# Performance work log

Hardware: AMD Instinct MI355X
Metric: run time of the kernel (lower is better)

Reference implementation:

```python
import jax, jax.numpy as jnp
import numpy as np

MAX_REL = 127  # default max_relative_position of NEZHA-style RelativePositionsEncoding


def rel_pos_encoding(L, d):
    """Clipped relative-distance sinusoidal encoding, shape [L, L, d]."""
    vocab = 2 * MAX_REL + 1
    pos = np.arange(vocab, dtype=np.float32)[:, None]
    i = np.arange(d)
    div = np.power(10000.0, (2 * (i // 2)) / d).astype(np.float32)
    ang = pos / div
    table = np.where(i % 2 == 0, np.sin(ang), np.cos(ang)).astype(np.float32)  # [vocab, d]
    dist = np.clip(np.arange(L)[None, :] - np.arange(L)[:, None], -MAX_REL, MAX_REL) + MAX_REL
    return jnp.asarray(table[dist])  # [L, L, d]


def setup_inputs() -> dict:
    key = jax.random.key(0)
    ks = jax.random.split(key, 5)
    B, L, H, C = 2, 256, 256, 5
    return {
        "hidden_state": jax.random.normal(ks[0], (B, L, H), dtype=jnp.float32),
        "mask": jnp.ones((B, L), dtype=jnp.int32),
        "Wh_w": jax.random.normal(ks[1], (4 * H, H), dtype=jnp.float32) * 0.02,
        "Wh_b": jax.random.normal(ks[2], (H,), dtype=jnp.float32) * 0.02,
        "Wo_w": jax.random.normal(ks[3], (H, C), dtype=jnp.float32) * 0.02,
        "Wo_b": jax.random.normal(ks[4], (C,), dtype=jnp.float32) * 0.02,
    }


def reference(hidden_state, mask, Wh_w, Wh_b, Wo_w, Wo_b):
    B, L, H = hidden_state.shape
    # Decompose Wh over the concat [end, start, end-start, end*start]:
    # Wh(cat) = end@(We+Wd) + start@(Ws-Wd) + (end*start)@Wm + rel@Wh + b  (exact, linearity)
    We, Ws, Wd, Wm = jnp.split(Wh_w, 4, axis=0)  # each [H, H]
    rel = rel_pos_encoding(L, 4 * H)                        # [L, L, 4H]
    rel_term = jnp.einsum('ijk,kh->ijh', rel, Wh_w)         # [L, L, H]
    a = hidden_state @ (We + Wd)                            # end-index contribution  [B, L, H]
    b = hidden_state @ (Ws - Wd)                            # start-index contribution [B, L, H]
    prod = hidden_state[:, :, None, :] * hidden_state[:, None, :, :]  # [B, L, L, H]
    pre = a[:, :, None, :] + b[:, None, :, :] + prod @ Wm + rel_term[None] + Wh_b
    hij = jnp.tanh(pre)                                     # [B, L, L, H]
    logits = hij @ Wo_w + Wo_b                              # [B, L, L, C]
    logits = jnp.transpose(logits, (0, 3, 1, 2))            # [B, C, L, L]
    m = mask.astype(bool)
    bad = (~m[:, None, :, None]) | (~m[:, None, None, :])
    logits = jnp.where(bad, -jnp.inf, logits)
    tri = jnp.tril(jnp.ones((L, L), logits.dtype), -1) * 1e12
    return logits - tri
```

## Files before the change

kernel.cpp:

```cpp
#include <hip/hip_runtime.h>
#include <math.h>

typedef _Float16 half8 __attribute__((ext_vector_type(8)));
typedef _Float16 half4v __attribute__((ext_vector_type(4)));
typedef float floatx4 __attribute__((ext_vector_type(4)));

union U16 { uint4 u; half8 h; };

__global__ __launch_bounds__(256) void k_prep1(
    const float* __restrict__ hs, const float* __restrict__ Wh,
    const float* __restrict__ Wo,
    float* __restrict__ Rp, float* __restrict__ ap, float* __restrict__ bp,
    uint4* __restrict__ WmT2, uint4* __restrict__ WoPk)
{
  __shared__ __align__(16) char pool[32768];
  int bid = blockIdx.x, tid = threadIdx.x;

  if (bid < 256) {
    float (*tbl)[8] = (float(*)[8])pool;
    int dg = bid >> 3, kq = bid & 7, d0 = dg * 8, k0 = kq * 128;
    for (int idx = tid; idx < 1024; idx += 256) {
      int t = idx >> 3, dl = idx & 7;
      int k = k0 + t;
      float e = (float)(k & ~1) * (1.0f / 1024.f);
      float div = powf(10000.f, e);
      float ang = (float)(d0 + dl) / div;
      tbl[t][dl] = (k & 1) ? cosf(ang) : sinf(ang);
    }
    __syncthreads();
    int h = tid;
    float acc[8] = {0, 0, 0, 0, 0, 0, 0, 0};
    for (int kk = 0; kk < 128; ++kk) {
      float wv = Wh[(k0 + kk) * 256 + h];
      float tr[8];
      *(float4*)&tr[0] = *(const float4*)&tbl[kk][0];
      *(float4*)&tr[4] = *(const float4*)&tbl[kk][4];
#pragma unroll
      for (int dl = 0; dl < 8; ++dl) acc[dl] = fmaf(tr[dl], wv, acc[dl]);
    }
#pragma unroll
    for (int dl = 0; dl < 8; ++dl)
      Rp[kq * 65536 + (d0 + dl) * 256 + h] = acc[dl];

  } else if (bid < 512) {
    float (*xs)[8] = (float(*)[8])pool;
    int g = bid - 256, rg = g >> 2, kq = g & 3;
    int r0 = rg * 8, k0 = kq * 64;
    for (int idx = tid; idx < 512; idx += 256) {
      int kk = idx >> 3, r = idx & 7;
      xs[kk][r] = hs[(r0 + r) * 256 + k0 + kk];
    }
    __syncthreads();
    int h = tid;
    float aa[8] = {0, 0, 0, 0, 0, 0, 0, 0}, bb[8] = {0, 0, 0, 0, 0, 0, 0, 0};
    for (int kk = 0; kk < 64; ++kk) {
      int k = k0 + kk;
      float we = Wh[k * 256 + h];
      float wsv = Wh[(256 + k) * 256 + h];
      float wd = Wh[(512 + k) * 256 + h];
      float wA = we + wd, wB = wsv - wd;
      float xr[8];
      *(float4*)&xr[0] = *(const float4*)&xs[kk][0];
      *(float4*)&xr[4] = *(const float4*)&xs[kk][4];
#pragma unroll
      for (int r = 0; r < 8; ++r) {
        aa[r] = fmaf(xr[r], wA, aa[r]);
        bb[r] = fmaf(xr[r], wB, bb[r]);
      }
    }
#pragma unroll
    for (int r = 0; r < 8; ++r) {
      ap[kq * 131072 + (r0 + r) * 256 + h] = aa[r];
      bp[kq * 131072 + (r0 + r) * 256 + h] = bb[r];
    }

  } else if (bid < 516) {
    _Float16 (*T)[256] = (_Float16(*)[256])pool;
    int q = bid - 512;
    for (int idx = tid; idx < 16384; idx += 256) {
      int k = idx >> 8, h = idx & 255;
      T[k][h] = (_Float16)Wh[(768 + q * 64 + k) * 256 + h];
    }
    __syncthreads();
    for (int gi = tid; gi < 2048; gi += 256) {
      int kbl = gi >> 8, h = gi & 255;
      U16 v;
#pragma unroll
      for (int e = 0; e < 8; ++e) v.h[e] = T[kbl * 8 + e][h];
      WmT2[(q * 8 + kbl) * 256 + h] = v.u;
    }

  } else {
    for (int gi = tid; gi < 512; gi += 256) {
      int kb = gi >> 4, c = gi & 15;
      U16 v;
#pragma unroll
      for (int e = 0; e < 8; ++e)
        v.h[e] = (c < 5) ? (_Float16)Wo[(kb * 8 + e) * 5 + c] : (_Float16)0.f;
      WoPk[gi] = v.u;
    }
  }
}

__global__ __launch_bounds__(256) void k_prep2(
    const float* __restrict__ Rp, const float* __restrict__ ap,
    const float* __restrict__ bp,
    float* __restrict__ R, float* __restrict__ a, float* __restrict__ bv)
{
  int bid = blockIdx.x, h = threadIdx.x;
  if (bid < 255) {
    int d = bid;
    float s = 0.f;
#pragma unroll
    for (int kq = 0; kq < 8; ++kq) s += Rp[kq * 65536 + d * 256 + h];
    R[d * 256 + h] = s;
  } else {
    int r0 = (bid - 255) * 2;
#pragma unroll
    for (int rr = 0; rr < 2; ++rr) {
      int r = r0 + rr;
      float sa = 0.f, sb = 0.f;
#pragma unroll
      for (int kq = 0; kq < 4; ++kq) {
        sa += ap[kq * 131072 + r * 256 + h];
        sb += bp[kq * 131072 + r * 256 + h];
      }
      a[r * 256 + h] = sa;
      bv[r * 256 + h] = sb;
    }
  }
}

__global__ __launch_bounds__(256, 4) void k_main(
    const float* __restrict__ hs, const int* __restrict__ mask,
    const float* __restrict__ R, const float* __restrict__ a,
    const float* __restrict__ bvec, const float* __restrict__ Whb,
    const uint4* __restrict__ WmT2, const uint4* __restrict__ WoPk,
    const float* __restrict__ Wob, float* __restrict__ out)
{
  __shared__ __align__(16) char smem[34304];
  _Float16 (*As)[264] = (_Float16(*)[264])smem;
  float (*stg)[268] = (float(*)[268])smem;

  int bid = blockIdx.x, tid = threadIdx.x;
  int jt = bid & 3, i = (bid >> 2) & 255, b = bid >> 10;
  int j0 = jt * 64;
  int lane = tid & 63, w = tid >> 6;
  int c16 = lane & 15, quad = lane >> 4;
  const float* hsb = hs + (size_t)b * 65536;

  float av[4];
#pragma unroll
  for (int ht2 = 0; ht2 < 4; ++ht2) {
    int hp = 64 * w + 16 * ht2 + c16;
    av[ht2] = a[((size_t)(b * 256 + i)) * 256 + hp] + Whb[hp];
  }

  floatx4 acc[4][4];
#pragma unroll
  for (int hf = 0; hf < 2; ++hf) {
    int jbase = j0 + hf * 32;
#pragma unroll
    for (int it = 0; it < 8; ++it) {
      int idx = it * 256 + tid;
      int row = idx >> 6;
      int c4 = (idx & 63) << 2;
      int jg = jbase + row;
      int dd = jg - i;
      dd = dd < -127 ? -127 : (dd > 127 ? 127 : dd);
      dd += 127;
      float4 bb = *(const float4*)(bvec + ((size_t)(b * 256 + jg)) * 256 + c4);
      float4 rr = *(const float4*)(R + (size_t)dd * 256 + c4);
      float4 s;
      s.x = bb.x + rr.x; s.y = bb.y + rr.y;
      s.z = bb.z + rr.z; s.w = bb.w + rr.w;
      *(float4*)&stg[row][c4] = s;
    }
    __syncthreads();
#pragma unroll
    for (int jj = 0; jj < 2; ++jj) {
      int jt2 = hf * 2 + jj;
#pragma unroll
      for (int r = 0; r < 4; ++r) {
        int jl32 = jj * 16 + quad * 4 + r;
#pragma unroll
        for (int ht2 = 0; ht2 < 4; ++ht2)
          acc[jt2][ht2][r] = av[ht2] + stg[jl32][64 * w + 16 * ht2 + c16];
      }
    }
    __syncthreads();
  }

  {
    int k8 = (tid & 31) * 8;
    float4 xi0 = *(const float4*)(hsb + i * 256 + k8);
    float4 xi1 = *(const float4*)(hsb + i * 256 + k8 + 4);
    int j = tid >> 5;
#pragma unroll
    for (int s = 0; s < 8; ++s, j += 8) {
      float4 xj0 = *(const float4*)(hsb + (j0 + j) * 256 + k8);
      float4 xj1 = *(const float4*)(hsb + (j0 + j) * 256 + k8 + 4);
      half8 p = {(_Float16)(xi0.x * xj0.x), (_Float16)(xi0.y * xj0.y),
                 (_Float16)(xi0.z * xj0.z), (_Float16)(xi0.w * xj0.w),
                 (_Float16)(xi1.x * xj1.x), (_Float16)(xi1.y * xj1.y),
                 (_Float16)(xi1.z * xj1.z), (_Float16)(xi1.w * xj1.w)};
      *(half8*)(&As[j][k8]) = p;
    }
  }
  __syncthreads();

#pragma unroll 1
  for (int kc = 0; kc < 4; ++kc) {
#pragma unroll
    for (int ks = 0; ks < 2; ++ks) {
      int kb = kc * 8 + ks * 4 + quad;
      U16 bg[4];
#pragma unroll
      for (int ht2 = 0; ht2 < 4; ++ht2)
        bg[ht2].u = WmT2[kb * 256 + 64 * w + 16 * ht2 + c16];
      half8 af[4];
#pragma unroll
      for (int jt2 = 0; jt2 < 4; ++jt2)
        af[jt2] = *(const half8*)(&As[jt2 * 16 + c16][kc * 64 + ks * 32 + quad * 8]);
#pragma unroll
      for (int jt2 = 0; jt2 < 4; ++jt2)
#pragma unroll
        for (int ht2 = 0; ht2 < 4; ++ht2)
          acc[jt2][ht2] = __builtin_amdgcn_mfma_f32_16x16x32_f16(
              af[jt2], bg[ht2].h, acc[jt2][ht2], 0, 0, 0);
    }
  }

  __syncthreads();

#pragma unroll
  for (int jt2 = 0; jt2 < 4; ++jt2) {
#pragma unroll
    for (int ht2 = 0; ht2 < 4; ++ht2) {
      int hp = 64 * w + 16 * ht2 + c16;
#pragma unroll
      for (int r = 0; r < 4; ++r) {
        int jl = jt2 * 16 + quad * 4 + r;
        float x = acc[jt2][ht2][r];
        float e = __expf(2.f * x);
        float t = fmaf(-2.f, __builtin_amdgcn_rcpf(e + 1.f), 1.f);
        As[jl][hp] = (_Float16)t;
      }
    }
  }
  __syncthreads();

  {
    U16 wog[8];
#pragma unroll
    for (int s = 0; s < 8; ++s) wog[s].u = WoPk[(s * 4 + quad) * 16 + c16];
    floatx4 accE = {0.f, 0.f, 0.f, 0.f};
#pragma unroll
    for (int s = 0; s < 8; ++s) {
      half8 ae = *(const half8*)(&As[16 * w + c16][s * 32 + quad * 8]);
      accE = __builtin_amdgcn_mfma_f32_16x16x32_f16(ae, wog[s].h, accE, 0, 0, 0);
    }
    const int* mb = mask + b * 256;
    int mi = mb[i];
    int jg0 = j0 + 16 * w + quad * 4;
    int mj[4];
    *(int4*)mj = *(const int4*)(mb + jg0);
    float wob = (c16 < 5) ? Wob[c16] : 0.f;
    float4 v;
#pragma unroll
    for (int r = 0; r < 4; ++r) {
      int jg = jg0 + r;
      float x = accE[r] + wob;
      if (!(mi && mj[r])) x = -INFINITY;
      if (jg < i) x -= 1e12f;
      ((float*)&v)[r] = x;
    }
    if (c16 < 5)
      *(float4*)(&out[(((size_t)b * 5 + c16) * 256 + i) * 256 + jg0]) = v;
  }
}

extern "C" void kernel_launch(void* const* d_in, const int* in_sizes, int n_in,
                              void* d_out, int out_size, void* d_ws, size_t ws_size,
                              hipStream_t stream) {
  const float* hs   = (const float*)d_in[0];
  const int*   mask = (const int*)d_in[1];
  const float* Wh_w = (const float*)d_in[2];
  const float* Wh_b = (const float*)d_in[3];
  const float* Wo_w = (const float*)d_in[4];
  const float* Wo_b = (const float*)d_in[5];

  char* ws = (char*)d_ws;
  float* R    = (float*)(ws + 0);
  float* a    = (float*)(ws + 262144);
  float* bv   = (float*)(ws + 786432);
  uint4* WmT2 = (uint4*)(ws + 1310720);
  uint4* WoPk = (uint4*)(ws + 1441792);
  float* Rp   = (float*)(ws + 1449984);
  float* ap   = (float*)(ws + 3547136);
  float* bp   = (float*)(ws + 5644288);

  k_prep1<<<517, 256, 0, stream>>>(hs, Wh_w, Wo_w, Rp, ap, bp, WmT2, WoPk);
  k_prep2<<<511, 256, 0, stream>>>(Rp, ap, bp, R, a, bv);
  k_main<<<2048, 256, 0, stream>>>(hs, mask, R, a, bv, Wh_b, WmT2, WoPk, Wo_b,
                                   (float*)d_out);
}
```

Baseline: 110.8 us.

## Drop split-K partials and merge the two prep kernels into one

The relative-position projection and the a/b projections now reduce over the full K dimension inside each block and write final results directly. This removes the partial-sum buffers and the separate reduction kernel, saving one launch and the round trip through global memory. In exchange, each R block streams all 1024 Wh rows per thread with a single serial accumulator, and the a/b pass uses fewer, longer-running blocks. That lowers parallelism and raises per-thread load traffic in the prep stage.

```diff
diff --git a/kernel.cpp b/kernel.cpp
--- a/kernel.cpp
+++ b/kernel.cpp
@@ -7,76 +7,73 @@
 
 union U16 { uint4 u; half8 h; };
 
-__global__ __launch_bounds__(256) void k_prep1(
+__global__ __launch_bounds__(256) void k_prep(
     const float* __restrict__ hs, const float* __restrict__ Wh,
     const float* __restrict__ Wo,
-    float* __restrict__ Rp, float* __restrict__ ap, float* __restrict__ bp,
+    float* __restrict__ R, float* __restrict__ a, float* __restrict__ bv,
     uint4* __restrict__ WmT2, uint4* __restrict__ WoPk)
 {
   __shared__ __align__(16) char pool[32768];
   int bid = blockIdx.x, tid = threadIdx.x;
 
   if (bid < 256) {
-    float (*tbl)[8] = (float(*)[8])pool;
-    int dg = bid >> 3, kq = bid & 7, d0 = dg * 8, k0 = kq * 128;
-    for (int idx = tid; idx < 1024; idx += 256) {
-      int t = idx >> 3, dl = idx & 7;
-      int k = k0 + t;
+    float* tbl = (float*)pool;
+    int d = bid;
+#pragma unroll
+    for (int s = 0; s < 4; ++s) {
+      int k = s * 256 + tid;
       float e = (float)(k & ~1) * (1.0f / 1024.f);
       float div = powf(10000.f, e);
-      float ang = (float)(d0 + dl) / div;
-      tbl[t][dl] = (k & 1) ? cosf(ang) : sinf(ang);
+      float ang = (float)d / div;
+      tbl[k] = (k & 1) ? cosf(ang) : sinf(ang);
     }
     __syncthreads();
     int h = tid;
-    float acc[8] = {0, 0, 0, 0, 0, 0, 0, 0};
-    for (int kk = 0; kk < 128; ++kk) {
-      float wv = Wh[(k0 + kk) * 256 + h];
-      float tr[8];
-      *(float4*)&tr[0] = *(const float4*)&tbl[kk][0];
-      *(float4*)&tr[4] = *(const float4*)&tbl[kk][4];
-#pragma unroll
-      for (int dl = 0; dl < 8; ++dl) acc[dl] = fmaf(tr[dl], wv, acc[dl]);
-    }
-#pragma unroll
-    for (int dl = 0; dl < 8; ++dl)
-      Rp[kq * 65536 + (d0 + dl) * 256 + h] = acc[dl];
-
-  } else if (bid < 512) {
-    float (*xs)[8] = (float(*)[8])pool;
-    int g = bid - 256, rg = g >> 2, kq = g & 3;
-    int r0 = rg * 8, k0 = kq * 64;
-    for (int idx = tid; idx < 512; idx += 256) {
-      int kk = idx >> 3, r = idx & 7;
-      xs[kk][r] = hs[(r0 + r) * 256 + k0 + kk];
+    float acc = 0.f;
+#pragma unroll 8
+    for (int k = 0; k < 1024; ++k)
+      acc = fmaf(tbl[k], Wh[k * 256 + h], acc);
+    R[d * 256 + h] = acc;
+
+  } else if (bid < 384) {
+    float (*xs)[260] = (float(*)[260])pool;
+    int r0 = (bid - 256) * 4;
+    {
+      int row = tid >> 6, c4 = (tid & 63) << 2;
+      float4 v = *(const float4*)(hs + (size_t)(r0 + row) * 256 + c4);
+      *(float4*)&xs[row][c4] = v;
     }
     __syncthreads();
     int h = tid;
-    float aa[8] = {0, 0, 0, 0, 0, 0, 0, 0}, bb[8] = {0, 0, 0, 0, 0, 0, 0, 0};
-    for (int kk = 0; kk < 64; ++kk) {
-      int k = k0 + kk;
-      float we = Wh[k * 256 + h];
-      float wsv = Wh[(256 + k) * 256 + h];
-      float wd = Wh[(512 + k) * 256 + h];
-      float wA = we + wd, wB = wsv - wd;
-      float xr[8];
-      *(float4*)&xr[0] = *(const float4*)&xs[kk][0];
-      *(float4*)&xr[4] = *(const float4*)&xs[kk][4];
-#pragma unroll
-      for (int r = 0; r < 8; ++r) {
-        aa[r] = fmaf(xr[r], wA, aa[r]);
-        bb[r] = fmaf(xr[r], wB, bb[r]);
+    float aa[4] = {0, 0, 0, 0}, bb[4] = {0, 0, 0, 0};
+    for (int k4 = 0; k4 < 256; k4 += 4) {
+      float4 xr[4];
+#pragma unroll
+      for (int r = 0; r < 4; ++r) xr[r] = *(const float4*)&xs[r][k4];
+#pragma unroll
+      for (int e = 0; e < 4; ++e) {
+        int k = k4 + e;
+        float we = Wh[k * 256 + h];
+        float wsv = Wh[(256 + k) * 256 + h];
+        float wd = Wh[(512 + k) * 256 + h];
+        float wA = we + wd, wB = wsv - wd;
+#pragma unroll
+        for (int r = 0; r < 4; ++r) {
+          float x = ((const float*)&xr[r])[e];
+          aa[r] = fmaf(x, wA, aa[r]);
+          bb[r] = fmaf(x, wB, bb[r]);
+        }
       }
     }
 #pragma unroll
-    for (int r = 0; r < 8; ++r) {
-      ap[kq * 131072 + (r0 + r) * 256 + h] = aa[r];
-      bp[kq * 131072 + (r0 + r) * 256 + h] = bb[r];
-    }
-
-  } else if (bid < 516) {
+    for (int r = 0; r < 4; ++r) {
+      a[(size_t)(r0 + r) * 256 + h] = aa[r];
+      bv[(size_t)(r0 + r) * 256 + h] = bb[r];
+    }
+
+  } else if (bid < 388) {
     _Float16 (*T)[256] = (_Float16(*)[256])pool;
-    int q = bid - 512;
+    int q = bid - 384;
     for (int idx = tid; idx < 16384; idx += 256) {
       int k = idx >> 8, h = idx & 255;
       T[k][h] = (_Float16)Wh[(768 + q * 64 + k) * 256 + h];
@@ -98,35 +95,6 @@
       for (int e = 0; e < 8; ++e)
         v.h[e] = (c < 5) ? (_Float16)Wo[(kb * 8 + e) * 5 + c] : (_Float16)0.f;
       WoPk[gi] = v.u;
-    }
-  }
-}
-
-__global__ __launch_bounds__(256) void k_prep2(
-    const float* __restrict__ Rp, const float* __restrict__ ap,
-    const float* __restrict__ bp,
-    float* __restrict__ R, float* __restrict__ a, float* __restrict__ bv)
-{
-  int bid = blockIdx.x, h = threadIdx.x;
-  if (bid < 255) {
-    int d = bid;
-    float s = 0.f;
-#pragma unroll
-    for (int kq = 0; kq < 8; ++kq) s += Rp[kq * 65536 + d * 256 + h];
-    R[d * 256 + h] = s;
-  } else {
-    int r0 = (bid - 255) * 2;
-#pragma unroll
-    for (int rr = 0; rr < 2; ++rr) {
-      int r = r0 + rr;
-      float sa = 0.f, sb = 0.f;
-#pragma unroll
-      for (int kq = 0; kq < 4; ++kq) {
-        sa += ap[kq * 131072 + r * 256 + h];
-        sb += bp[kq * 131072 + r * 256 + h];
-      }
-      a[r * 256 + h] = sa;
-      bv[r * 256 + h] = sb;
     }
   }
 }
@@ -296,12 +264,8 @@
   float* bv   = (float*)(ws + 786432);
   uint4* WmT2 = (uint4*)(ws + 1310720);
   uint4* WoPk = (uint4*)(ws + 1441792);
-  float* Rp   = (float*)(ws + 1449984);
-  float* ap   = (float*)(ws + 3547136);
-  float* bp   = (float*)(ws + 5644288);
-
-  k_prep1<<<517, 256, 0, stream>>>(hs, Wh_w, Wo_w, Rp, ap, bp, WmT2, WoPk);
-  k_prep2<<<511, 256, 0, stream>>>(Rp, ap, bp, R, a, bv);
+
+  k_prep<<<389, 256, 0, stream>>>(hs, Wh_w, Wo_w, R, a, bv, WmT2, WoPk);
   k_main<<<2048, 256, 0, stream>>>(hs, mask, R, a, bv, Wh_b, WmT2, WoPk, Wo_b,
                                    (float*)d_out);
 }
```

Result: slower. 133.2 us (+20.2%).
